# Optimization experiments

Hardware: AMD Instinct MI355X
Metric: run time of the kernel (lower is better)

Reference implementation:

```python
import jax, jax.numpy as jnp
import numpy as np

N = 100000   # nodes
E = 300000   # directed edges (avg degree 3, molecular graphs)
G = 4000     # molecules in the batch
IN = 9
HID = 128
HEADS = 4
NEG_SLOPE = 0.2


def setup_inputs() -> dict:
    key = jax.random.key(0)
    ks = jax.random.split(key, 12)
    x = jax.random.normal(ks[0], (N, IN), dtype=jnp.float32)
    edge_index = jax.random.randint(ks[1], (2, E), 0, N, dtype=jnp.int32)
    batch = jnp.sort(jax.random.randint(ks[2], (N,), 0, G, dtype=jnp.int32))
    s = 0.1  # keep activations in a sane range
    W1 = jax.random.normal(ks[3], (IN, HEADS * HID), dtype=jnp.float32) * s
    a_src1 = jax.random.normal(ks[4], (HEADS, HID), dtype=jnp.float32) * s
    a_dst1 = jax.random.normal(ks[5], (HEADS, HID), dtype=jnp.float32) * s
    b1 = jax.random.normal(ks[6], (HEADS * HID,), dtype=jnp.float32) * s
    W2 = jax.random.normal(ks[7], (HEADS * HID, HID), dtype=jnp.float32) * s
    a_src2 = jax.random.normal(ks[8], (1, HID), dtype=jnp.float32) * s
    a_dst2 = jax.random.normal(ks[9], (1, HID), dtype=jnp.float32) * s
    b2 = jax.random.normal(ks[10], (HID,), dtype=jnp.float32) * s
    return {"x": x, "edge_index": edge_index, "batch": batch,
            "W1": W1, "a_src1": a_src1, "a_dst1": a_dst1, "b1": b1,
            "W2": W2, "a_src2": a_src2, "a_dst2": a_dst2, "b2": b2}


def _gat_conv(x, edge_index, W, a_src, a_dst, b, heads, out_ch, concat):
    """PyG GATConv: linear proj, per-edge leaky-relu attention logits,
    segment softmax over destination nodes, scatter-add aggregation.
    add_self_loops=True (PyG default)."""
    n = x.shape[0]
    loops = jnp.arange(n, dtype=edge_index.dtype)
    src = jnp.concatenate([edge_index[0], loops])
    dst = jnp.concatenate([edge_index[1], loops])

    h = (x @ W).reshape(n, heads, out_ch)                  # [N, H, C]
    alpha_s = jnp.einsum('nhc,hc->nh', h, a_src)           # [N, H]
    alpha_d = jnp.einsum('nhc,hc->nh', h, a_dst)           # [N, H]

    logits = jax.nn.leaky_relu(alpha_s[src] + alpha_d[dst], NEG_SLOPE)  # [Etot, H]
    # numerically stable segment softmax over incoming edges of each dst
    m = jax.ops.segment_max(logits, dst, num_segments=n)   # [N, H] (finite: self-loops)
    e = jnp.exp(logits - m[dst])
    z = jax.ops.segment_sum(e, dst, num_segments=n)
    alpha = e / (z[dst] + 1e-16)                           # [Etot, H]

    msg = h[src] * alpha[:, :, None]                       # [Etot, H, C]
    out = jax.ops.segment_sum(msg, dst, num_segments=n)    # [N, H, C]
    if concat:
        out = out.reshape(n, heads * out_ch)
    else:
        out = out.mean(axis=1)
    return out + b


def reference(x, edge_index, batch, W1, a_src1, a_dst1, b1, W2, a_src2, a_dst2, b2):
    h = jax.nn.elu(_gat_conv(x, edge_index, W1, a_src1, a_dst1, b1, HEADS, HID, True))
    h = jax.nn.elu(_gat_conv(h, edge_index, W2, a_src2, a_dst2, b2, 1, HID, True))
    # global mean pool per graph
    sums = jax.ops.segment_sum(h, batch, num_segments=G)   # [G, HID]
    cnt = jax.ops.segment_sum(jnp.ones((h.shape[0],), h.dtype), batch, num_segments=G)
    return sums / jnp.maximum(cnt, 1.0)[:, None]
```

## Files before the change

kernel.cpp:

```cpp
#include <hip/hip_runtime.h>

#define N_NODES 100000
#define N_EDGES 300000
#define N_GRAPHS 4000
#define CAP 32

typedef float f32x4 __attribute__((ext_vector_type(4)));
typedef __bf16 bf16x8 __attribute__((ext_vector_type(8)));
typedef __bf16 bf16x2 __attribute__((ext_vector_type(2)));
typedef _Float16 f16x2 __attribute__((ext_vector_type(2)));
typedef _Float16 f16x8 __attribute__((ext_vector_type(8)));

__device__ __forceinline__ float fdot2f16(f16x2 a, f16x2 b, float c) {
#if __has_builtin(__builtin_amdgcn_fdot2)
    return __builtin_amdgcn_fdot2(a, b, c, false);
#else
    return c + (float)a.x * (float)b.x + (float)a.y * (float)b.y;
#endif
}

static const size_t OFF_XA    = 0;
static const size_t OFF_AD4   = OFF_XA + (size_t)N_NODES * 16;
static const size_t OFF_P2B   = OFF_AD4 + (size_t)N_NODES * 4;
static const size_t OFF_ASAD2 = OFF_P2B + (size_t)N_NODES * 64;
static const size_t OFF_H3B   = OFF_ASAD2 + (size_t)N_NODES * 2;
static const size_t OFF_WSB   = OFF_H3B + (size_t)N_NODES * 64;
static const size_t OFF_W1H   = OFF_WSB + 32768;
static const size_t OFF_GST   = OFF_W1H + 2560;
static const size_t OFF_INT   = OFF_GST + 4096;

#define PRE_NODE_END 391
#define PRE_PACKB_END 455
#define PRE_W1H_END 465
#define PRE_DEG_END 856
#define PRE_GST_END 872

__device__ __forceinline__ float lrelu(float x) { return x < 0.f ? 0.2f * x : x; }
__device__ __forceinline__ float elu(float x)   { return x > 0.f ? x : __expf(x) - 1.f; }

__global__ __launch_bounds__(256) void k_pre(
    const float* __restrict__ x, const float* __restrict__ W1,
    const float* __restrict__ a_src1, const float* __restrict__ a_dst1,
    const float* __restrict__ W2, const int* __restrict__ batch,
    float* __restrict__ xa, float* __restrict__ ad4,
    __bf16* __restrict__ wsB, f16x2* __restrict__ w1h,
    int* __restrict__ deg, int* __restrict__ gstart) {
    int b = blockIdx.x, tid = threadIdx.x;
    if (b < PRE_NODE_END) {
        __shared__ float wf[72];
        if (tid < 72) {
            int isd = tid / 36, r = tid % 36, k = r / 4, h = r % 4;
            const float* a = isd ? a_dst1 : a_src1;
            float s = 0.f;
            for (int c = 0; c < 128; c++) s += W1[k * 512 + h * 128 + c] * a[h * 128 + c];
            wf[tid] = s;
        }
        __syncthreads();
        int n = b * 256 + tid;
        if (n >= N_NODES) return;
        float xv[9];
#pragma unroll
        for (int k = 0; k < 9; k++) xv[k] = x[n * 9 + k];
        float as[4], ad[4];
#pragma unroll
        for (int h = 0; h < 4; h++) {
            float s = 0.f, d = 0.f;
#pragma unroll
            for (int k = 0; k < 9; k++) {
                s += xv[k] * wf[k * 4 + h];
                d += xv[k] * wf[36 + k * 4 + h];
            }
            as[h] = s; ad[h] = d;
        }
        f32x4* xp = (f32x4*)(xa + (size_t)n * 16);
        xp[0] = (f32x4){xv[0], xv[1], xv[2], xv[3]};
        xp[1] = (f32x4){xv[4], xv[5], xv[6], xv[7]};
        xp[2] = (f32x4){xv[8], as[0], as[1], as[2]};
        xp[3] = (f32x4){as[3], 0.f, 0.f, 0.f};
        *(f32x4*)(ad4 + (size_t)n * 4) = (f32x4){ad[0], ad[1], ad[2], ad[3]};
    } else if (b < PRE_PACKB_END) {
        int t = (b - PRE_NODE_END) * 256 + tid;
#pragma unroll
        for (int m = 0; m < 4; m++) {
            int idx = t * 4 + m;
            int k = idx >> 7, nn = idx & 127;
            wsB[(size_t)nn * 512 + k] = (__bf16)W2[(size_t)k * 128 + nn];
        }
    } else if (b < PRE_W1H_END) {
        int t = (b - PRE_PACKB_END) * 256 + tid;
        if (t < 2560) {
            int p = t >> 9, j = t & 511;
            f16x2 v;
            v.x = (_Float16)W1[(2 * p) * 512 + j];
            v.y = (p < 4) ? (_Float16)W1[(2 * p + 1) * 512 + j] : (_Float16)0.f;
            w1h[t] = v;
        }
    } else if (b < PRE_DEG_END) {
        int idx = (b - PRE_W1H_END) * 256 + tid;
        if (idx < N_NODES) deg[idx] = 0;
    } else {
        int g = (b - PRE_DEG_END) * 256 + tid;
        if (g > N_GRAPHS) return;
        int lo = 0, hi = N_NODES;
        while (lo < hi) { int mid = (lo + hi) >> 1; if (batch[mid] < g) lo = mid + 1; else hi = mid; }
        gstart[g] = lo;
    }
}

__global__ void k_bucket(const int* __restrict__ ei, int* __restrict__ deg,
                         int* __restrict__ bucket) {
    int e = blockIdx.x * 256 + threadIdx.x;
    if (e >= N_EDGES) return;
    int s = ei[e], d = ei[N_EDGES + e];
    int slot = atomicAdd(&deg[d], 1);
    if (slot < CAP) bucket[d * CAP + slot] = s;
}

__global__ __launch_bounds__(512, 6) void k_gemm(
    const float* __restrict__ xa, const float* __restrict__ ad4,
    const int* __restrict__ deg, const int* __restrict__ bucket,
    const f16x2* __restrict__ w1h, const float* __restrict__ b1,
    const __bf16* __restrict__ wsB,
    const float* __restrict__ a_src2, const float* __restrict__ a_dst2,
    __bf16* __restrict__ p2b, float* __restrict__ asad2) {
    __shared__ __bf16 As[64 * 256];
    __shared__ _Float16 AgT[64 * 72];
    __shared__ float red2[64 * 16];
    const int tid = threadIdx.x;
    const int lane = tid & 63;
    const int w = tid >> 6;
    const int i = lane & 15;
    const int q = lane >> 4;
    const int m0 = blockIdx.x * 64;

    {
        int nh = tid >> 1, sub = tid & 1;
        int r = nh >> 2, h = nh & 3;
        int n = m0 + r;
        float acc[9] = {};
        float z = 0.f;
        bool valid = (n < N_NODES);
        if (valid) {
            float ad = ad4[(size_t)n * 4 + h];
            int dg = deg[n];
            if (dg > CAP) dg = CAP;
            if (sub == 0) {
                const f32x4* xp = (const f32x4*)(xa + (size_t)n * 16);
                f32x4 v0 = xp[0], v1 = xp[1], v2 = xp[2], v3 = xp[3];
                float asl = (h == 0) ? v2.y : (h == 1) ? v2.z : (h == 2) ? v2.w : v3.x;
                float e = __expf(lrelu(asl + ad));
                z += e;
                acc[0] += e * v0.x; acc[1] += e * v0.y; acc[2] += e * v0.z; acc[3] += e * v0.w;
                acc[4] += e * v1.x; acc[5] += e * v1.y; acc[6] += e * v1.z; acc[7] += e * v1.w;
                acc[8] += e * v2.x;
            }
            for (int j = sub; j < dg; j += 2) {
                int src = bucket[n * CAP + j];
                const f32x4* xp = (const f32x4*)(xa + (size_t)src * 16);
                f32x4 v0 = xp[0], v1 = xp[1], v2 = xp[2], v3 = xp[3];
                float asl = (h == 0) ? v2.y : (h == 1) ? v2.z : (h == 2) ? v2.w : v3.x;
                float e = __expf(lrelu(asl + ad));
                z += e;
                acc[0] += e * v0.x; acc[1] += e * v0.y; acc[2] += e * v0.z; acc[3] += e * v0.w;
                acc[4] += e * v1.x; acc[5] += e * v1.y; acc[6] += e * v1.z; acc[7] += e * v1.w;
                acc[8] += e * v2.x;
            }
        }
        z += __shfl_xor(z, 1);
#pragma unroll
        for (int k = 0; k < 9; k++) acc[k] += __shfl_xor(acc[k], 1);
        if (sub == 0) {
            float inv = valid ? 1.f / z : 0.f;
            f16x8 p0;
#pragma unroll
            for (int k = 0; k < 8; k++) p0[k] = (_Float16)(acc[k] * inv);
            _Float16* dst = AgT + r * 72 + h * 16;
            *(f16x8*)dst = p0;
            dst[8] = (_Float16)(acc[8] * inv);
        }
    }
    __syncthreads();

    f32x4 acc[4];
#pragma unroll
    for (int r = 0; r < 4; r++) acc[r] = (f32x4){0.f, 0.f, 0.f, 0.f};

    const int row = tid & 63;
    const int kg = __builtin_amdgcn_readfirstlane(tid >> 6);
    const int rt_p1 = row >> 4, il = row & 15;
    const __bf16* bcol = wsB + (size_t)(w * 16 + i) * 512 + q * 8;

#pragma unroll
    for (int half = 0; half < 2; half++) {
        bf16x8 breg[8];
#pragma unroll
        for (int kc = 0; kc < 8; kc++)
            breg[kc] = *(const bf16x8*)(bcol + half * 256 + kc * 32);

        {
            int h = half * 2 + (kg >> 2);
            f16x2 agp[5];
            {
                const _Float16* ab = &AgT[row * 72 + h * 16];
#pragma unroll
                for (int p = 0; p < 4; p++) agp[p] = *(const f16x2*)(ab + 2 * p);
                agp[4].x = ab[8];
                agp[4].y = (_Float16)0.f;
            }
#pragma unroll
            for (int c8 = 0; c8 < 4; c8++) {
                int j0 = half * 256 + kg * 32 + c8 * 8;
                float o[8];
#pragma unroll
                for (int e = 0; e < 8; e++) o[e] = b1[j0 + e];
#pragma unroll
                for (int p = 0; p < 5; p++) {
                    const f16x2* wp = w1h + p * 512 + j0;
#pragma unroll
                    for (int e = 0; e < 8; e++) o[e] = fdot2f16(agp[p], wp[e], o[e]);
                }
                bf16x8 pk;
#pragma unroll
                for (int e = 0; e < 8; e++) pk[e] = (__bf16)elu(o[e]);
                *(bf16x8*)&As[(rt_p1 * 8 + kg) * 512 + (c8 * 16 + il) * 8] = pk;
            }
        }
        __syncthreads();

#pragma unroll
        for (int kc = 0; kc < 8; kc++) {
#pragma unroll
            for (int rt = 0; rt < 4; rt++) {
                bf16x8 af = *(const bf16x8*)&As[(rt * 8 + kc) * 512 + lane * 8];
                acc[rt] = __builtin_amdgcn_mfma_f32_16x16x32_bf16(af, breg[kc], acc[rt], 0, 0, 0);
            }
        }
        __syncthreads();
    }

    float as2 = a_src2[w * 16 + i];
    float ad2 = a_dst2[w * 16 + i];
#pragma unroll
    for (int rt = 0; rt < 4; rt++) {
#pragma unroll
        for (int qq = 0; qq < 4; qq++) {
            int r2 = rt * 16 + q * 4 + qq;
            float v = acc[rt][qq];
            if (m0 + r2 < N_NODES)
                p2b[(size_t)(m0 + r2) * 128 + w * 16 + i] = (__bf16)v;
            float s = v * as2, d = v * ad2;
#pragma unroll
            for (int off = 1; off < 16; off <<= 1) {
                s += __shfl_xor(s, off);
                d += __shfl_xor(d, off);
            }
            if (i == 0) {
                red2[r2 * 16 + w * 2] = s;
                red2[r2 * 16 + w * 2 + 1] = d;
            }
        }
    }
    __syncthreads();
    if (tid < 128) {
        int r2 = tid >> 1, cc = tid & 1;
        float sum = 0.f;
#pragma unroll
        for (int ww = 0; ww < 8; ww++) sum += red2[r2 * 16 + ww * 2 + cc];
        if (m0 + r2 < N_NODES) asad2[(size_t)(m0 + r2) * 2 + cc] = sum;
    }
}

__global__ void k_agg2(const __bf16* __restrict__ p2b, const float* __restrict__ asad2,
                       const int* __restrict__ deg, const int* __restrict__ bucket,
                       const float* __restrict__ b2, __bf16* __restrict__ h3b) {
    int n = (blockIdx.x * 256 + threadIdx.x) >> 6;
    n = __builtin_amdgcn_readfirstlane(n);
    if (n >= N_NODES) return;
    int lane = threadIdx.x & 63;
    float ad = asad2[n * 2 + 1];
    float e = __expf(lrelu(asad2[n * 2] + ad));
    float z = e;
    bf16x2 v = ((const bf16x2*)(p2b + (size_t)n * 128))[lane];
    float a0 = e * (float)v.x;
    float a1 = e * (float)v.y;
    int dg = deg[n];
    if (dg > CAP) dg = CAP;
    for (int j = 0; j < dg; j += 4) {
        int s0 = bucket[n * CAP + j];
        int s1 = bucket[n * CAP + min(j + 1, dg - 1)];
        int s2 = bucket[n * CAP + min(j + 2, dg - 1)];
        int s3 = bucket[n * CAP + min(j + 3, dg - 1)];
        float l0 = asad2[s0 * 2], l1 = asad2[s1 * 2];
        float l2 = asad2[s2 * 2], l3 = asad2[s3 * 2];
        bf16x2 w0 = ((const bf16x2*)(p2b + (size_t)s0 * 128))[lane];
        bf16x2 w1 = ((const bf16x2*)(p2b + (size_t)s1 * 128))[lane];
        bf16x2 w2 = ((const bf16x2*)(p2b + (size_t)s2 * 128))[lane];
        bf16x2 w3 = ((const bf16x2*)(p2b + (size_t)s3 * 128))[lane];
        float e0 = __expf(lrelu(l0 + ad));
        float e1 = (j + 1 < dg) ? __expf(lrelu(l1 + ad)) : 0.f;
        float e2 = (j + 2 < dg) ? __expf(lrelu(l2 + ad)) : 0.f;
        float e3 = (j + 3 < dg) ? __expf(lrelu(l3 + ad)) : 0.f;
        z += e0 + e1 + e2 + e3;
        a0 += e0 * (float)w0.x + e1 * (float)w1.x + e2 * (float)w2.x + e3 * (float)w3.x;
        a1 += e0 * (float)w0.y + e1 * (float)w1.y + e2 * (float)w2.y + e3 * (float)w3.y;
    }
    float inv = 1.f / z;
    bf16x2 o;
    o.x = (__bf16)elu(a0 * inv + b2[2 * lane]);
    o.y = (__bf16)elu(a1 * inv + b2[2 * lane + 1]);
    ((bf16x2*)(h3b + (size_t)n * 128))[lane] = o;
}

__global__ void k_pool(const __bf16* __restrict__ h3b, const int* __restrict__ gstart,
                       float* __restrict__ out) {
    int g = (blockIdx.x * 256 + threadIdx.x) >> 6;
    g = __builtin_amdgcn_readfirstlane(g);
    if (g >= N_GRAPHS) return;
    int lane = threadIdx.x & 63;
    int s = gstart[g], e = gstart[g + 1];
    float a0 = 0.f, a1 = 0.f;
    for (int n = s; n < e; n++) {
        bf16x2 v = ((const bf16x2*)(h3b + (size_t)n * 128))[lane];
        a0 += (float)v.x;
        a1 += (float)v.y;
    }
    int cnt = e - s;
    float ic = (cnt > 0) ? 1.f / (float)cnt : 0.f;
    out[(size_t)g * 128 + 2 * lane] = a0 * ic;
    out[(size_t)g * 128 + 2 * lane + 1] = a1 * ic;
}

extern "C" void kernel_launch(void* const* d_in, const int* in_sizes, int n_in,
                              void* d_out, int out_size, void* d_ws, size_t ws_size,
                              hipStream_t stream) {
    const float* x       = (const float*)d_in[0];
    const int*   ei      = (const int*)d_in[1];
    const int*   batch   = (const int*)d_in[2];
    const float* W1      = (const float*)d_in[3];
    const float* a_src1  = (const float*)d_in[4];
    const float* a_dst1  = (const float*)d_in[5];
    const float* b1      = (const float*)d_in[6];
    const float* W2      = (const float*)d_in[7];
    const float* a_src2  = (const float*)d_in[8];
    const float* a_dst2  = (const float*)d_in[9];
    const float* b2      = (const float*)d_in[10];
    float* out = (float*)d_out;

    float* wsf   = (float*)d_ws;
    float* xa    = wsf + OFF_XA;
    float* ad4   = wsf + OFF_AD4;
    __bf16* p2b  = (__bf16*)(wsf + OFF_P2B);
    float* asad2 = wsf + OFF_ASAD2;
    __bf16* h3b  = (__bf16*)(wsf + OFF_H3B);
    __bf16* wsB  = (__bf16*)(wsf + OFF_WSB);
    f16x2* w1h   = (f16x2*)(wsf + OFF_W1H);
    int* gstart  = (int*)(wsf + OFF_GST);
    int* wsi    = (int*)(wsf + OFF_INT);
    int* deg    = wsi;
    int* bucket = wsi + N_NODES;

    k_pre<<<PRE_GST_END, 256, 0, stream>>>(x, W1, a_src1, a_dst1, W2, batch,
                                           xa, ad4, wsB, w1h, deg, gstart);
    k_bucket<<<(N_EDGES + 255) / 256, 256, 0, stream>>>(ei, deg, bucket);
    k_gemm<<<(N_NODES + 63) / 64, 512, 0, stream>>>(xa, ad4, deg, bucket, w1h, b1,
                                                    wsB, a_src2, a_dst2, p2b, asad2);
    k_agg2<<<((size_t)N_NODES * 64 + 255) / 256, 256, 0, stream>>>(
        p2b, asad2, deg, bucket, b2, h3b);
    k_pool<<<(N_GRAPHS * 64) / 256, 256, 0, stream>>>(h3b, gstart, out);
}
```

Baseline: 212.3 us.

## Fuse layer-2 aggregation with mean pooling and fold bucketing into pre kernel

After: 195.3 us. 1.09x faster.

```diff
diff --git a/kernel.cpp b/kernel.cpp
--- a/kernel.cpp
+++ b/kernel.cpp
@@ -23,8 +23,7 @@
 static const size_t OFF_AD4   = OFF_XA + (size_t)N_NODES * 16;
 static const size_t OFF_P2B   = OFF_AD4 + (size_t)N_NODES * 4;
 static const size_t OFF_ASAD2 = OFF_P2B + (size_t)N_NODES * 64;
-static const size_t OFF_H3B   = OFF_ASAD2 + (size_t)N_NODES * 2;
-static const size_t OFF_WSB   = OFF_H3B + (size_t)N_NODES * 64;
+static const size_t OFF_WSB   = OFF_ASAD2 + (size_t)N_NODES * 2;
 static const size_t OFF_W1H   = OFF_WSB + 32768;
 static const size_t OFF_GST   = OFF_W1H + 2560;
 static const size_t OFF_INT   = OFF_GST + 4096;
@@ -32,8 +31,8 @@
 #define PRE_NODE_END 391
 #define PRE_PACKB_END 455
 #define PRE_W1H_END 465
-#define PRE_DEG_END 856
-#define PRE_GST_END 872
+#define PRE_GST_END 481
+#define PRE_BKT_END 1653
 
 __device__ __forceinline__ float lrelu(float x) { return x < 0.f ? 0.2f * x : x; }
 __device__ __forceinline__ float elu(float x)   { return x > 0.f ? x : __expf(x) - 1.f; }
@@ -42,9 +41,10 @@
     const float* __restrict__ x, const float* __restrict__ W1,
     const float* __restrict__ a_src1, const float* __restrict__ a_dst1,
     const float* __restrict__ W2, const int* __restrict__ batch,
+    const int* __restrict__ ei,
     float* __restrict__ xa, float* __restrict__ ad4,
     __bf16* __restrict__ wsB, f16x2* __restrict__ w1h,
-    int* __restrict__ deg, int* __restrict__ gstart) {
+    int* __restrict__ deg, int* __restrict__ bucket, int* __restrict__ gstart) {
     int b = blockIdx.x, tid = threadIdx.x;
     if (b < PRE_NODE_END) {
         __shared__ float wf[72];
@@ -95,25 +95,19 @@
             v.y = (p < 4) ? (_Float16)W1[(2 * p + 1) * 512 + j] : (_Float16)0.f;
             w1h[t] = v;
         }
-    } else if (b < PRE_DEG_END) {
-        int idx = (b - PRE_W1H_END) * 256 + tid;
-        if (idx < N_NODES) deg[idx] = 0;
-    } else {
-        int g = (b - PRE_DEG_END) * 256 + tid;
+    } else if (b < PRE_GST_END) {
+        int g = (b - PRE_W1H_END) * 256 + tid;
         if (g > N_GRAPHS) return;
         int lo = 0, hi = N_NODES;
         while (lo < hi) { int mid = (lo + hi) >> 1; if (batch[mid] < g) lo = mid + 1; else hi = mid; }
         gstart[g] = lo;
-    }
-}
-
-__global__ void k_bucket(const int* __restrict__ ei, int* __restrict__ deg,
-                         int* __restrict__ bucket) {
-    int e = blockIdx.x * 256 + threadIdx.x;
-    if (e >= N_EDGES) return;
-    int s = ei[e], d = ei[N_EDGES + e];
-    int slot = atomicAdd(&deg[d], 1);
-    if (slot < CAP) bucket[d * CAP + slot] = s;
+    } else {
+        int e = (b - PRE_GST_END) * 256 + tid;
+        if (e >= N_EDGES) return;
+        int s = ei[e], d = ei[N_EDGES + e];
+        int slot = atomicAdd(&deg[d], 1);
+        if (slot < CAP) bucket[d * CAP + slot] = s;
+    }
 }
 
 __global__ __launch_bounds__(512, 6) void k_gemm(
@@ -270,64 +264,59 @@
     }
 }
 
-__global__ void k_agg2(const __bf16* __restrict__ p2b, const float* __restrict__ asad2,
-                       const int* __restrict__ deg, const int* __restrict__ bucket,
-                       const float* __restrict__ b2, __bf16* __restrict__ h3b) {
-    int n = (blockIdx.x * 256 + threadIdx.x) >> 6;
-    n = __builtin_amdgcn_readfirstlane(n);
-    if (n >= N_NODES) return;
-    int lane = threadIdx.x & 63;
-    float ad = asad2[n * 2 + 1];
-    float e = __expf(lrelu(asad2[n * 2] + ad));
-    float z = e;
-    bf16x2 v = ((const bf16x2*)(p2b + (size_t)n * 128))[lane];
-    float a0 = e * (float)v.x;
-    float a1 = e * (float)v.y;
-    int dg = deg[n];
-    if (dg > CAP) dg = CAP;
-    for (int j = 0; j < dg; j += 4) {
-        int s0 = bucket[n * CAP + j];
-        int s1 = bucket[n * CAP + min(j + 1, dg - 1)];
-        int s2 = bucket[n * CAP + min(j + 2, dg - 1)];
-        int s3 = bucket[n * CAP + min(j + 3, dg - 1)];
-        float l0 = asad2[s0 * 2], l1 = asad2[s1 * 2];
-        float l2 = asad2[s2 * 2], l3 = asad2[s3 * 2];
-        bf16x2 w0 = ((const bf16x2*)(p2b + (size_t)s0 * 128))[lane];
-        bf16x2 w1 = ((const bf16x2*)(p2b + (size_t)s1 * 128))[lane];
-        bf16x2 w2 = ((const bf16x2*)(p2b + (size_t)s2 * 128))[lane];
-        bf16x2 w3 = ((const bf16x2*)(p2b + (size_t)s3 * 128))[lane];
-        float e0 = __expf(lrelu(l0 + ad));
-        float e1 = (j + 1 < dg) ? __expf(lrelu(l1 + ad)) : 0.f;
-        float e2 = (j + 2 < dg) ? __expf(lrelu(l2 + ad)) : 0.f;
-        float e3 = (j + 3 < dg) ? __expf(lrelu(l3 + ad)) : 0.f;
-        z += e0 + e1 + e2 + e3;
-        a0 += e0 * (float)w0.x + e1 * (float)w1.x + e2 * (float)w2.x + e3 * (float)w3.x;
-        a1 += e0 * (float)w0.y + e1 * (float)w1.y + e2 * (float)w2.y + e3 * (float)w3.y;
-    }
-    float inv = 1.f / z;
-    bf16x2 o;
-    o.x = (__bf16)elu(a0 * inv + b2[2 * lane]);
-    o.y = (__bf16)elu(a1 * inv + b2[2 * lane + 1]);
-    ((bf16x2*)(h3b + (size_t)n * 128))[lane] = o;
-}
-
-__global__ void k_pool(const __bf16* __restrict__ h3b, const int* __restrict__ gstart,
-                       float* __restrict__ out) {
-    int g = (blockIdx.x * 256 + threadIdx.x) >> 6;
-    g = __builtin_amdgcn_readfirstlane(g);
-    if (g >= N_GRAPHS) return;
-    int lane = threadIdx.x & 63;
-    int s = gstart[g], e = gstart[g + 1];
-    float a0 = 0.f, a1 = 0.f;
-    for (int n = s; n < e; n++) {
-        bf16x2 v = ((const bf16x2*)(h3b + (size_t)n * 128))[lane];
-        a0 += (float)v.x;
-        a1 += (float)v.y;
-    }
-    int cnt = e - s;
-    float ic = (cnt > 0) ? 1.f / (float)cnt : 0.f;
-    out[(size_t)g * 128 + 2 * lane] = a0 * ic;
-    out[(size_t)g * 128 + 2 * lane + 1] = a1 * ic;
+__global__ __launch_bounds__(256) void k_agg2pool(
+    const __bf16* __restrict__ p2b, const float* __restrict__ asad2,
+    const int* __restrict__ deg, const int* __restrict__ bucket,
+    const float* __restrict__ b2, const int* __restrict__ gstart,
+    float* __restrict__ out) {
+    __shared__ float red[4 * 128];
+    int g = blockIdx.x;
+    int tid = threadIdx.x;
+    int wv = __builtin_amdgcn_readfirstlane(tid >> 6);
+    int lane = tid & 63;
+    int s0n = gstart[g], e0n = gstart[g + 1];
+    float b2a = b2[2 * lane], b2b = b2[2 * lane + 1];
+    float g0 = 0.f, g1 = 0.f;
+    for (int n = s0n + wv; n < e0n; n += 4) {
+        float ad = asad2[n * 2 + 1];
+        float e = __expf(lrelu(asad2[n * 2] + ad));
+        float z = e;
+        bf16x2 v = ((const bf16x2*)(p2b + (size_t)n * 128))[lane];
+        float a0 = e * (float)v.x;
+        float a1 = e * (float)v.y;
+        int dg = deg[n];
+        if (dg > CAP) dg = CAP;
+        for (int j = 0; j < dg; j += 4) {
+            int s0 = bucket[n * CAP + j];
+            int s1 = bucket[n * CAP + min(j + 1, dg - 1)];
+            int s2 = bucket[n * CAP + min(j + 2, dg - 1)];
+            int s3 = bucket[n * CAP + min(j + 3, dg - 1)];
+            float l0 = asad2[s0 * 2], l1 = asad2[s1 * 2];
+            float l2 = asad2[s2 * 2], l3 = asad2[s3 * 2];
+            bf16x2 w0 = ((const bf16x2*)(p2b + (size_t)s0 * 128))[lane];
+            bf16x2 w1 = ((const bf16x2*)(p2b + (size_t)s1 * 128))[lane];
+            bf16x2 w2 = ((const bf16x2*)(p2b + (size_t)s2 * 128))[lane];
+            bf16x2 w3 = ((const bf16x2*)(p2b + (size_t)s3 * 128))[lane];
+            float e0 = __expf(lrelu(l0 + ad));
+            float e1 = (j + 1 < dg) ? __expf(lrelu(l1 + ad)) : 0.f;
+            float e2 = (j + 2 < dg) ? __expf(lrelu(l2 + ad)) : 0.f;
+            float e3 = (j + 3 < dg) ? __expf(lrelu(l3 + ad)) : 0.f;
+            z += e0 + e1 + e2 + e3;
+            a0 += e0 * (float)w0.x + e1 * (float)w1.x + e2 * (float)w2.x + e3 * (float)w3.x;
+            a1 += e0 * (float)w0.y + e1 * (float)w1.y + e2 * (float)w2.y + e3 * (float)w3.y;
+        }
+        float inv = 1.f / z;
+        g0 += elu(a0 * inv + b2a);
+        g1 += elu(a1 * inv + b2b);
+    }
+    red[wv * 128 + 2 * lane] = g0;
+    red[wv * 128 + 2 * lane + 1] = g1;
+    __syncthreads();
+    if (tid < 128) {
+        float sum = red[tid] + red[128 + tid] + red[256 + tid] + red[384 + tid];
+        int cnt = e0n - s0n;
+        out[(size_t)g * 128 + tid] = sum / (float)(cnt > 0 ? cnt : 1);
+    }
 }
 
 extern "C" void kernel_launch(void* const* d_in, const int* in_sizes, int n_in,
@@ -351,7 +340,6 @@
     float* ad4   = wsf + OFF_AD4;
     __bf16* p2b  = (__bf16*)(wsf + OFF_P2B);
     float* asad2 = wsf + OFF_ASAD2;
-    __bf16* h3b  = (__bf16*)(wsf + OFF_H3B);
     __bf16* wsB  = (__bf16*)(wsf + OFF_WSB);
     f16x2* w1h   = (f16x2*)(wsf + OFF_W1H);
     int* gstart  = (int*)(wsf + OFF_GST);
@@ -359,12 +347,10 @@
     int* deg    = wsi;
     int* bucket = wsi + N_NODES;
 
-    k_pre<<<PRE_GST_END, 256, 0, stream>>>(x, W1, a_src1, a_dst1, W2, batch,
-                                           xa, ad4, wsB, w1h, deg, gstart);
-    k_bucket<<<(N_EDGES + 255) / 256, 256, 0, stream>>>(ei, deg, bucket);
+    hipMemsetAsync(deg, 0, N_NODES * sizeof(int), stream);
+    k_pre<<<PRE_BKT_END, 256, 0, stream>>>(x, W1, a_src1, a_dst1, W2, batch, ei,
+                                           xa, ad4, wsB, w1h, deg, bucket, gstart);
     k_gemm<<<(N_NODES + 63) / 64, 512, 0, stream>>>(xa, ad4, deg, bucket, w1h, b1,
                                                     wsB, a_src2, a_dst2, p2b, asad2);
-    k_agg2<<<((size_t)N_NODES * 64 + 255) / 256, 256, 0, stream>>>(
-        p2b, asad2, deg, bucket, b2, h3b);
-    k_pool<<<(N_GRAPHS * 64) / 256, 256, 0, stream>>>(h3b, gstart, out);
-}
+    k_agg2pool<<<N_GRAPHS, 256, 0, stream>>>(p2b, asad2, deg, bucket, b2, gstart, out);
+}
```
